# Optimization experiments

Measured on AMD Instinct MI355X. Metric: run time of the kernel, lower is better.

## Reference

```python
import jax, jax.numpy as jnp
import numpy as np

N_LAYERS, D_MODEL, H, D_K, D_V, D_FF, VOCAB = 6, 512, 8, 64, 64, 2048, 32000
B, S = 4, 512
NEG_INF = -jnp.inf


def positional_encoding(seq_len, d_model):
    # Faithful to the (buggy-vs-paper) source: angle = pos / 10000**(2*i/d_model),
    # sin for even i, cos for odd i (i is the raw channel index).
    pos = jnp.arange(seq_len, dtype=jnp.float32)[:, None]
    i = jnp.arange(d_model, dtype=jnp.float32)[None, :]
    angle = pos / jnp.power(10000.0, 2.0 * i / d_model)
    return jnp.where((jnp.arange(d_model) % 2 == 0)[None, :], jnp.sin(angle), jnp.cos(angle))


def layer_norm(x, g, b, eps=1e-5):
    mu = jnp.mean(x, -1, keepdims=True)
    var = jnp.mean((x - mu) ** 2, -1, keepdims=True)
    return (x - mu) * jax.lax.rsqrt(var + eps) * g + b


def mha(q_in, k_in, v_in, wq, wk, wv, wo, q_mask, k_mask, causal):
    # wq/wk: (H, D, D_K), wv: (H, D, D_V), wo: (H*D_V, D)
    q = jnp.einsum('bsd,hdk->bhsk', q_in, wq)
    k = jnp.einsum('btd,hdk->bhtk', k_in, wk)
    v = jnp.einsum('btd,hdk->bhtk', v_in, wv)
    scores = jnp.einsum('bhsk,bhtk->bhst', q, k) / jnp.sqrt(jnp.float32(D_K))
    allowed = q_mask[:, None, :, None] & k_mask[:, None, None, :]  # (B,1,S,T)
    if causal:
        sl, tl = q_in.shape[1], k_in.shape[1]
        allowed = allowed & (jnp.arange(tl)[None, :] <= jnp.arange(sl)[:, None])[None, None]
    scores = jnp.where(allowed, scores, NEG_INF)
    attn = jax.nn.softmax(scores, axis=-1)
    out = jnp.einsum('bhst,bhtk->bshk', attn, v)  # (B,S,H,D_V)
    out = out.reshape(out.shape[0], out.shape[1], H * D_V)
    return out @ wo


def ffn(x, w1, b1, w2, b2):
    return jax.nn.relu(x @ w1 + b1) @ w2 + b2


def setup_inputs() -> dict:
    key = jax.random.key(0)
    ks = iter(jax.random.split(key, 40))
    f = lambda shape, scale: (jax.random.normal(next(ks), shape, dtype=jnp.float32) * scale)
    inp = {
        'src_tokens': jax.random.randint(next(ks), (B, S), 0, VOCAB),
        'tgt_tokens': jax.random.randint(next(ks), (B, S), 0, VOCAB),
        'src_mask': jnp.ones((B, S), dtype=bool),
        'tgt_mask': jnp.ones((B, S), dtype=bool),
        'embed': f((VOCAB, D_MODEL), 0.02),
        'enc_wqkv': f((N_LAYERS, 3, H, D_MODEL, D_K), 0.04),
        'enc_wo': f((N_LAYERS, H * D_V, D_MODEL), 0.04),
        'enc_ff_w1': f((N_LAYERS, D_MODEL, D_FF), 0.02),
        'enc_ff_b1': jnp.zeros((N_LAYERS, D_FF), jnp.float32),
        'enc_ff_w2': f((N_LAYERS, D_FF, D_MODEL), 0.02),
        'enc_ff_b2': jnp.zeros((N_LAYERS, D_MODEL), jnp.float32),
        'enc_ln_g': jnp.ones((N_LAYERS, 2, D_MODEL), jnp.float32),
        'enc_ln_b': jnp.zeros((N_LAYERS, 2, D_MODEL), jnp.float32),
        'dec_wqkv1': f((N_LAYERS, 3, H, D_MODEL, D_K), 0.04),
        'dec_wo1': f((N_LAYERS, H * D_V, D_MODEL), 0.04),
        'dec_wqkv2': f((N_LAYERS, 3, H, D_MODEL, D_K), 0.04),
        'dec_wo2': f((N_LAYERS, H * D_V, D_MODEL), 0.04),
        'dec_ff_w1': f((N_LAYERS, D_MODEL, D_FF), 0.02),
        'dec_ff_b1': jnp.zeros((N_LAYERS, D_FF), jnp.float32),
        'dec_ff_w2': f((N_LAYERS, D_FF, D_MODEL), 0.02),
        'dec_ff_b2': jnp.zeros((N_LAYERS, D_MODEL), jnp.float32),
        'dec_ln_g': jnp.ones((N_LAYERS, 3, D_MODEL), jnp.float32),
        'dec_ln_b': jnp.zeros((N_LAYERS, 3, D_MODEL), jnp.float32),
        'out_w': f((D_MODEL, VOCAB), 0.02),
        'out_b': jnp.zeros((VOCAB,), jnp.float32),
    }
    return inp


def reference(src_tokens, tgt_tokens, src_mask, tgt_mask, embed,
              enc_wqkv, enc_wo, enc_ff_w1, enc_ff_b1, enc_ff_w2, enc_ff_b2, enc_ln_g, enc_ln_b,
              dec_wqkv1, dec_wo1, dec_wqkv2, dec_wo2, dec_ff_w1, dec_ff_b1, dec_ff_w2, dec_ff_b2,
              dec_ln_g, dec_ln_b, out_w, out_b):
    pe = positional_encoding(src_tokens.shape[1], D_MODEL)
    x = embed[src_tokens] + pe[None]
    for i in range(N_LAYERS):
        a = mha(x, x, x, enc_wqkv[i, 0], enc_wqkv[i, 1], enc_wqkv[i, 2], enc_wo[i], src_mask, src_mask, False)
        x = layer_norm(x + a, enc_ln_g[i, 0], enc_ln_b[i, 0])
        x = layer_norm(x + ffn(x, enc_ff_w1[i], enc_ff_b1[i], enc_ff_w2[i], enc_ff_b2[i]), enc_ln_g[i, 1], enc_ln_b[i, 1])
    pe_t = positional_encoding(tgt_tokens.shape[1], D_MODEL)
    y = embed[tgt_tokens] + pe_t[None]
    for i in range(N_LAYERS):
        a = mha(y, y, y, dec_wqkv1[i, 0], dec_wqkv1[i, 1], dec_wqkv1[i, 2], dec_wo1[i], tgt_mask, tgt_mask, True)
        y = layer_norm(y + a, dec_ln_g[i, 0], dec_ln_b[i, 0])
        a = mha(y, x, x, dec_wqkv2[i, 0], dec_wqkv2[i, 1], dec_wqkv2[i, 2], dec_wo2[i], tgt_mask, src_mask, False)
        y = layer_norm(y + a, dec_ln_g[i, 1], dec_ln_b[i, 1])
        y = layer_norm(y + ffn(y, dec_ff_w1[i], dec_ff_b1[i], dec_ff_w2[i], dec_ff_b2[i]), dec_ln_g[i, 2], dec_ln_b[i, 2])
    return y @ out_w + out_b
```

## Files before the change

### kernel.cpp

```cpp
#include <hip/hip_runtime.h>
#include <math.h>


typedef unsigned short u16;
typedef __attribute__((ext_vector_type(8))) short short8;
typedef __attribute__((ext_vector_type(4))) float f32x4;

__device__ __forceinline__ u16 f2bf(float f){
  unsigned u = __float_as_uint(f);
  return (u16)((u + 0x7fffu + ((u >> 16) & 1u)) >> 16);
}

#define GLDS16(gp, lp) __builtin_amdgcn_global_load_lds( \
    (const __attribute__((address_space(1))) unsigned int*)(const void*)(gp), \
    (__attribute__((address_space(3))) unsigned int*)(void*)(lp), 16, 0, 0)

__global__ __launch_bounds__(256) void embed_dual_kernel(
    const int* __restrict__ src, const int* __restrict__ tgt,
    const float* __restrict__ emb,
    float* __restrict__ xb, u16* __restrict__ xh,
    float* __restrict__ yb, u16* __restrict__ yh)
{
  int which = blockIdx.x >> 11;
  int row = blockIdx.x & 2047;
  int s = row & 511;
  int t = which ? tgt[row] : src[row];
  float* out = which ? yb : xb;
  u16*  outh = which ? yh : xh;
  #pragma unroll
  for (int j = 0; j < 2; j++){
    int d = threadIdx.x + 256*j;
    float ang = (float)s * powf(10000.0f, -2.0f*(float)d/512.0f);
    float pe = (d & 1) ? cosf(ang) : sinf(ang);
    float v = emb[(size_t)t*512 + d] + pe;
    out[(size_t)row*512 + d] = v;
    outh[(size_t)row*512 + d] = f2bf(v);
  }
}

struct WDesc { const float* W; unsigned long long gs, ds; u16* dst; int K; int nx; int end; };
struct WPack { WDesc d[6]; };

__device__ __forceinline__ void cast_body(const WPack& P, int nseg, int blk){
  __shared__ u16 T[64][65];
  int s = 0;
  while (s < nseg-1 && blk >= P.d[s].end) s++;
  WDesc D = P.d[s];
  int base = s ? P.d[s-1].end : 0;
  int lb = blk - base;
  int g = lb % D.nx, kt = lb / D.nx;
  int tid = threadIdx.x;
  const float* Wb = D.W + (size_t)g*D.gs + (size_t)kt*64*D.ds;
  #pragma unroll
  for (int i = 0; i < 16; i++){
    int li = tid + 256*i;
    int kk = li >> 6, c = li & 63;
    T[kk][c] = f2bf(Wb[(size_t)kk*D.ds + c]);
  }
  __syncthreads();
  #pragma unroll
  for (int i = 0; i < 16; i++){
    int lo = tid + 256*i;
    int c = lo >> 6, kk = lo & 63;
    D.dst[(size_t)(g*64 + c)*D.K + kt*64 + kk] = T[kk][c];
  }
}

__global__ __launch_bounds__(256) void wcast_multi(WPack P, int nseg){
  cast_body(P, nseg, blockIdx.x);
}

__device__ __forceinline__ void ln_body(
    float* __restrict__ x, const float* __restrict__ res,
    const float* __restrict__ g, const float* __restrict__ bt,
    u16* __restrict__ xh, int blk)
{
  int tid = threadIdx.x, lane = tid & 63, wv = tid >> 6;
  int row = blk*4 + wv;
  size_t base = (size_t)row*512;
  float v[8]; float sum = 0.f;
  #pragma unroll
  for (int j = 0; j < 8; j++){
    int d = lane + 64*j;
    v[j] = x[base + d] + res[base + d];
    sum += v[j];
  }
  #pragma unroll
  for (int o = 32; o; o >>= 1) sum += __shfl_xor(sum, o);
  float mu = sum * (1.0f/512.0f);
  float vs = 0.f;
  #pragma unroll
  for (int j = 0; j < 8; j++){ float dd = v[j] - mu; vs += dd*dd; }
  #pragma unroll
  for (int o = 32; o; o >>= 1) vs += __shfl_xor(vs, o);
  float rstd = rsqrtf(vs*(1.0f/512.0f) + 1e-5f);
  #pragma unroll
  for (int j = 0; j < 8; j++){
    int d = lane + 64*j;
    float ov = (v[j] - mu)*rstd*g[d] + bt[d];
    x[base + d] = ov;
    xh[base + d] = f2bf(ov);
  }
}

__global__ __launch_bounds__(256) void ln_cast_kernel(
    float* __restrict__ x, const float* __restrict__ res,
    const float* __restrict__ g, const float* __restrict__ bt,
    u16* __restrict__ xh, WPack P, int nseg)
{
  int bid = blockIdx.x;
  if (bid < 512){ ln_body(x, res, g, bt, xh, bid); return; }
  cast_body(P, nseg, bid - 512);
}

__global__ __launch_bounds__(256) void ln_kernel(
    float* __restrict__ x, const float* __restrict__ res,
    const float* __restrict__ g, const float* __restrict__ bt,
    u16* __restrict__ xh)
{
  ln_body(x, res, g, bt, xh, blockIdx.x);
}

__global__ __launch_bounds__(256) void flash_attn_kernel(
    const u16* __restrict__ qkv, const u16* __restrict__ vT,
    u16* __restrict__ ctx, int causal)
{
  __shared__ __align__(16) u16 lQ[64*64];
  __shared__ __align__(16) u16 lK[2][64*64];
  __shared__ __align__(16) u16 lV[2][64*64];
  __shared__ __align__(16) u16 lP[4][16*64];
  int tid = threadIdx.x, lane = tid & 63, w = tid >> 6;
  int r16 = lane & 15, l4 = lane >> 4;
  int bh = blockIdx.x >> 3, qb = blockIdx.x & 7;
  int b = bh >> 3, h = bh & 7;
  const u16* qbase = qkv + (size_t)b*512*1536 + h*64;

  #pragma unroll
  for (int i = 0; i < 2; i++){
    int idx = i*256 + tid;
    int r = idx >> 3, c = idx & 7;
    GLDS16(qbase + (size_t)(qb*64 + r)*1536 + ((c ^ (r & 7))*8),
           lQ + (i*256 + w*64)*8);
  }
  auto stageKV = [&](int buf, int tt){
    #pragma unroll
    for (int i = 0; i < 2; i++){
      int idx = i*256 + tid;
      int r = idx >> 3, c = idx & 7;
      GLDS16(qbase + 512 + (size_t)(tt*64 + r)*1536 + ((c ^ (r & 7))*8),
             lK[buf] + (i*256 + w*64)*8);
      GLDS16(vT + ((size_t)bh*64 + r)*512 + tt*64 + ((c ^ (r & 7))*8),
             lV[buf] + (i*256 + w*64)*8);
    }
  };
  stageKV(0, 0);
  __syncthreads();
  short8 qa[2];
  #pragma unroll
  for (int kt = 0; kt < 2; kt++){
    int q = w*16 + r16;
    qa[kt] = *(const short8*)&lQ[q*64 + (((kt*4 + l4) ^ (q & 7))*8)];
  }

  f32x4 o[4];
  float mrow[4], lrow[4];
  #pragma unroll
  for (int j = 0; j < 4; j++){ o[j] = (f32x4){0.f,0.f,0.f,0.f}; mrow[j] = -3e38f; lrow[j] = 0.f; }

  int ntl = causal ? (qb + 1) : 8;
  int buf = 0;
  for (int tt = 0; tt < ntl; tt++){
    if (tt + 1 < ntl) stageKV(buf ^ 1, tt + 1);
    f32x4 s[4];
    #pragma unroll
    for (int ct = 0; ct < 4; ct++) s[ct] = (f32x4){0.f,0.f,0.f,0.f};
    __builtin_amdgcn_s_setprio(1);
    #pragma unroll
    for (int kt = 0; kt < 2; kt++){
      #pragma unroll
      for (int ct = 0; ct < 4; ct++){
        int trow = ct*16 + r16;
        short8 kb = *(const short8*)&lK[buf][trow*64 + (((kt*4 + l4) ^ (trow & 7))*8)];
        s[ct] = __builtin_amdgcn_mfma_f32_16x16x32_bf16(qa[kt], kb, s[ct], 0, 0, 0);
      }
    }
    __builtin_amdgcn_s_setprio(0);
    float p[4][4];
    #pragma unroll
    for (int ct = 0; ct < 4; ct++)
      #pragma unroll
      for (int r = 0; r < 4; r++){
        float v = s[ct][r] * 0.125f;
        if (causal && tt == qb && (ct*16 + r16) > (w*16 + l4*4 + r)) v = -1e30f;
        p[ct][r] = v;
      }
    #pragma unroll
    for (int r = 0; r < 4; r++){
      float pm = fmaxf(fmaxf(p[0][r], p[1][r]), fmaxf(p[2][r], p[3][r]));
      #pragma unroll
      for (int off = 1; off < 16; off <<= 1) pm = fmaxf(pm, __shfl_xor(pm, off));
      float mn = fmaxf(mrow[r], pm);
      float scl = __expf(mrow[r] - mn);
      mrow[r] = mn;
      float rs = 0.f;
      #pragma unroll
      for (int ct = 0; ct < 4; ct++){ p[ct][r] = __expf(p[ct][r] - mn); rs += p[ct][r]; }
      #pragma unroll
      for (int off = 1; off < 16; off <<= 1) rs += __shfl_xor(rs, off);
      lrow[r] = lrow[r]*scl + rs;
      #pragma unroll
      for (int jf = 0; jf < 4; jf++) o[jf][r] *= scl;
    }
    u16* myP = &lP[w][0];
    #pragma unroll
    for (int ct = 0; ct < 4; ct++)
      #pragma unroll
      for (int r = 0; r < 4; r++){
        int q = l4*4 + r, t = ct*16 + r16;
        myP[q*64 + (((t >> 3) ^ (q & 7))*8) + (t & 7)] = f2bf(p[ct][r]);
      }
    __builtin_amdgcn_s_setprio(1);
    #pragma unroll
    for (int kt = 0; kt < 2; kt++){
      short8 pa = *(const short8*)&myP[r16*64 + (((kt*4 + l4) ^ (r16 & 7))*8)];
      #pragma unroll
      for (int jf = 0; jf < 4; jf++){
        int dr = jf*16 + r16;
        short8 vv = *(const short8*)&lV[buf][dr*64 + (((kt*4 + l4) ^ (dr & 7))*8)];
        o[jf] = __builtin_amdgcn_mfma_f32_16x16x32_bf16(pa, vv, o[jf], 0, 0, 0);
      }
    }
    __builtin_amdgcn_s_setprio(0);
    __syncthreads();
    buf ^= 1;
  }
  #pragma unroll
  for (int r = 0; r < 4; r++){
    float inv = 1.0f / lrow[r];
    int q = qb*64 + w*16 + l4*4 + r;
    u16* dst = ctx + (size_t)(b*512 + q)*512 + h*64;
    #pragma unroll
    for (int jf = 0; jf < 4; jf++)
      dst[jf*16 + r16] = f2bf(o[jf][r] * inv);
  }
}

template<int BM, int BN, int WM, int WN, int VOUT, int SWZ>
__global__ __launch_bounds__(WM*WN*64) void mfma_gemm(
    const u16* __restrict__ A, int lda,
    const u16* __restrict__ B, int ldb,
    void* __restrict__ C, int ldc, int cbf,
    const float* __restrict__ bias, int relu, int K, u16* __restrict__ vt)
{
  constexpr int NT  = WM*WN*64;
  constexpr int SM  = BM/WM, SN = BN/WN;
  constexpr int FM  = SM/16, FN = SN/16;
  constexpr int RPS = NT/8;
  constexpr int AG  = BM/RPS, BG = BN/RPS;
  __shared__ __align__(16) u16 lds[2][(BM+BN)*64];
  int bx, by;
  if constexpr (SWZ){
    int nwg = gridDim.x * gridDim.y;
    int lin = blockIdx.y * gridDim.x + blockIdx.x;
    int q = nwg >> 3, r = nwg & 7;
    int xcd = lin & 7, idx = lin >> 3;
    int wgid = (xcd < r ? xcd*(q+1) : r*(q+1) + (xcd-r)*q) + idx;
    bx = wgid / gridDim.y; by = wgid % gridDim.y;
  } else { bx = blockIdx.x; by = blockIdx.y; }
  int tid = threadIdx.x, lane = tid & 63, w = tid >> 6;
  int wm = w / WN, wn = w % WN;
  int r16 = lane & 15, l4 = lane >> 4;
  int sr = (w << 3) + (lane >> 3);
  int sc = lane & 7;
  int scs = sc ^ (sr & 7);
  const u16* Ab = A + (size_t)by*BM*lda + (size_t)sr*lda + scs*8;
  const u16* Bb = B + (size_t)bx*BN*ldb + (size_t)sr*ldb + scs*8;
  f32x4 acc[FM][FN];
  #pragma unroll
  for (int i = 0; i < FM; i++)
    #pragma unroll
    for (int j = 0; j < FN; j++)
      acc[i][j] = (f32x4){0.f, 0.f, 0.f, 0.f};

  auto stage = [&](int buf, int kt){
    #pragma unroll
    for (int s = 0; s < AG; s++)
      GLDS16(Ab + (size_t)(s*RPS)*lda + kt, &lds[buf][(s*RPS + (w << 3))*64]);
    #pragma unroll
    for (int s = 0; s < BG; s++)
      GLDS16(Bb + (size_t)(s*RPS)*ldb + kt, &lds[buf][(BM + s*RPS + (w << 3))*64]);
  };
  stage(0, 0);
  int nk = K >> 6, cur = 0;
  for (int kt = 0; kt < nk; kt++){
    __syncthreads();
    if (kt + 1 < nk) stage(cur ^ 1, (kt + 1) << 6);
    #pragma unroll
    for (int ks = 0; ks < 2; ks++){
      short8 av[FM], bv[FN];
      #pragma unroll
      for (int i = 0; i < FM; i++){
        int row = wm*SM + i*16 + r16;
        av[i] = *(const short8*)&lds[cur][row*64 + (((ks*4 + l4) ^ (row & 7))*8)];
      }
      #pragma unroll
      for (int j = 0; j < FN; j++){
        int row = wn*SN + j*16 + r16;
        bv[j] = *(const short8*)&lds[cur][(BM + row)*64 + (((ks*4 + l4) ^ (row & 7))*8)];
      }
      #pragma unroll
      for (int i = 0; i < FM; i++)
        #pragma unroll
        for (int j = 0; j < FN; j++)
          acc[i][j] = __builtin_amdgcn_mfma_f32_16x16x32_bf16(av[i], bv[j], acc[i][j], 0, 0, 0);
    }
    cur ^= 1;
  }

  if constexpr (VOUT){
    int nblk = bx * BN;
    if (nblk >= 1024){
      constexpr int TP = BM + 4;
      u16* T = &lds[0][0];
      __syncthreads();
      #pragma unroll
      for (int i = 0; i < FM; i++){
        int t0 = wm*SM + i*16 + l4*4;
        #pragma unroll
        for (int j = 0; j < FN; j++){
          int d = wn*SN + j*16 + r16;
          unsigned q01 = (unsigned)f2bf(acc[i][j][0]) | ((unsigned)f2bf(acc[i][j][1]) << 16);
          unsigned q23 = (unsigned)f2bf(acc[i][j][2]) | ((unsigned)f2bf(acc[i][j][3]) << 16);
          uint2 pk; pk.x = q01; pk.y = q23;
          *(uint2*)&T[d*TP + t0] = pk;
        }
      }
      __syncthreads();
      int h0 = (nblk - 1024) >> 6;
      int b = (by * BM) >> 9;
      int t0g = (by * BM) & 511;
      constexpr int U2PR = BM/4;
      constexpr int NIT = (BN*BM)/(NT*4);
      #pragma unroll
      for (int it = 0; it < NIT; it++){
        int idx = it*NT + tid;
        int d = idx / U2PR, tq = (idx % U2PR)*4;
        int hh = d >> 6, dd = d & 63;
        *(uint2*)&vt[((size_t)((b*8 + h0 + hh)*64 + dd))*512 + t0g + tq] =
            *(const uint2*)&T[d*TP + tq];
      }
      return;
    }
  }

  int m0 = by*BM + wm*SM, n0 = bx*BN + wn*SN;
  int r4 = l4*4;
  #pragma unroll
  for (int i = 0; i < FM; i++){
    #pragma unroll
    for (int j = 0; j < FN; j++){
      int col = n0 + j*16 + r16;
      float bi = bias ? bias[col] : 0.f;
      #pragma unroll
      for (int r = 0; r < 4; r++){
        int rowg = m0 + i*16 + r4 + r;
        float o = acc[i][j][r] + bi;
        if (relu) o = fmaxf(o, 0.f);
        if (cbf) ((u16*)C)[(size_t)rowg*ldc + col] = f2bf(o);
        else     ((float*)C)[(size_t)rowg*ldc + col] = o;
      }
    }
  }
}

__global__ __launch_bounds__(256) void xattn_qkv_gemm(
    const u16* __restrict__ Ay, const u16* __restrict__ Ax,
    const u16* __restrict__ Bt, u16* __restrict__ C, u16* __restrict__ vt)
{
  constexpr int BM=64, BN=64, WM=2, WN=2, NT=256;
  constexpr int SM=BM/WM, SN=BN/WN, FM=SM/16, FN=SN/16, RPS=NT/8;
  constexpr int AG=BM/RPS, BG=BN/RPS;
  __shared__ __align__(16) u16 lA[2][BM*64];
  __shared__ __align__(16) u16 lB[2][BN*64];
  int tid = threadIdx.x, lane = tid & 63, w = tid >> 6;
  int wm = w / WN, wn = w % WN;
  int r16 = lane & 15, l4 = lane >> 4;
  int sr = (w << 3) + (lane >> 3);
  int sc = lane & 7;
  int scs = sc ^ (sr & 7);
  int z = blockIdx.z;
  const u16* A = (z == 0) ? Ay : Ax;
  const u16* Ab = A + (size_t)blockIdx.y*BM*512 + (size_t)sr*512 + scs*8;
  const u16* Bb = Bt + (size_t)(z*512 + blockIdx.x*BN)*512 + (size_t)sr*512 + scs*8;
  f32x4 acc[FM][FN];
  #pragma unroll
  for (int i = 0; i < FM; i++)
    #pragma unroll
    for (int j = 0; j < FN; j++)
      acc[i][j] = (f32x4){0.f, 0.f, 0.f, 0.f};
  auto stage = [&](int buf, int kt){
    #pragma unroll
    for (int s = 0; s < AG; s++)
      GLDS16(Ab + (size_t)(s*RPS)*512 + kt, &lA[buf][(s*RPS + (w << 3))*64]);
    #pragma unroll
    for (int s = 0; s < BG; s++)
      GLDS16(Bb + (size_t)(s*RPS)*512 + kt, &lB[buf][(s*RPS + (w << 3))*64]);
  };
  stage(0, 0);
  int cur = 0;
  for (int kt = 0; kt < 8; kt++){
    __syncthreads();
    if (kt + 1 < 8) stage(cur ^ 1, (kt + 1) << 6);
    #pragma unroll
    for (int ks = 0; ks < 2; ks++){
      short8 av[FM], bv[FN];
      #pragma unroll
      for (int i = 0; i < FM; i++){
        int row = wm*SM + i*16 + r16;
        av[i] = *(const short8*)&lA[cur][row*64 + (((ks*4 + l4) ^ (row & 7))*8)];
      }
      #pragma unroll
      for (int j = 0; j < FN; j++){
        int row = wn*SN + j*16 + r16;
        bv[j] = *(const short8*)&lB[cur][row*64 + (((ks*4 + l4) ^ (row & 7))*8)];
      }
      #pragma unroll
      for (int i = 0; i < FM; i++)
        #pragma unroll
        for (int j = 0; j < FN; j++)
          acc[i][j] = __builtin_amdgcn_mfma_f32_16x16x32_bf16(av[i], bv[j], acc[i][j], 0, 0, 0);
    }
    cur ^= 1;
  }
  if (z == 2){
    constexpr int TP = BM + 4;
    u16* T = (u16*)&lA[0][0];
    __syncthreads();
    #pragma unroll
    for (int i = 0; i < FM; i++){
      int t0 = wm*SM + i*16 + l4*4;
      #pragma unroll
      for (int j = 0; j < FN; j++){
        int d = wn*SN + j*16 + r16;
        unsigned q01 = (unsigned)f2bf(acc[i][j][0]) | ((unsigned)f2bf(acc[i][j][1]) << 16);
        unsigned q23 = (unsigned)f2bf(acc[i][j][2]) | ((unsigned)f2bf(acc[i][j][3]) << 16);
        uint2 pk; pk.x = q01; pk.y = q23;
        *(uint2*)&T[d*TP + t0] = pk;
      }
    }
    __syncthreads();
    int h = blockIdx.x;
    int b = (blockIdx.y * BM) >> 9;
    int t0g = (blockIdx.y * BM) & 511;
    u16* dst = vt + (size_t)(b*8 + h)*64*512;
    #pragma unroll
    for (int it = 0; it < (BM*64)/(NT*4); it++){
      int idx = it*NT + tid;
      int d = idx >> 4, tq = (idx & 15)*4;
      *(uint2*)&dst[(size_t)d*512 + t0g + tq] = *(const uint2*)&T[d*TP + tq];
    }
    return;
  }
  int m0 = blockIdx.y*BM + wm*SM, n0 = z*512 + blockIdx.x*BN + wn*SN;
  int r4 = l4*4;
  #pragma unroll
  for (int i = 0; i < FM; i++)
    #pragma unroll
    for (int j = 0; j < FN; j++)
      #pragma unroll
      for (int r = 0; r < 4; r++){
        int rowg = m0 + i*16 + r4 + r;
        C[(size_t)rowg*1536 + n0 + j*16 + r16] = f2bf(acc[i][j][r]);
      }
}

extern "C" void kernel_launch(void* const* d_in, const int* in_sizes, int n_in,
                              void* d_out, int out_size, void* d_ws, size_t ws_size,
                              hipStream_t stream)
{
  (void)in_sizes; (void)n_in; (void)out_size; (void)ws_size;
  const int*   src_tok   = (const int*)  d_in[0];
  const int*   tgt_tok   = (const int*)  d_in[1];
  const float* emb       = (const float*)d_in[4];
  const float* enc_wqkv  = (const float*)d_in[5];
  const float* enc_wo    = (const float*)d_in[6];
  const float* enc_ff_w1 = (const float*)d_in[7];
  const float* enc_ff_b1 = (const float*)d_in[8];
  const float* enc_ff_w2 = (const float*)d_in[9];
  const float* enc_ff_b2 = (const float*)d_in[10];
  const float* enc_ln_g  = (const float*)d_in[11];
  const float* enc_ln_b  = (const float*)d_in[12];
  const float* dec_wqkv1 = (const float*)d_in[13];
  const float* dec_wo1   = (const float*)d_in[14];
  const float* dec_wqkv2 = (const float*)d_in[15];
  const float* dec_wo2   = (const float*)d_in[16];
  const float* dec_ff_w1 = (const float*)d_in[17];
  const float* dec_ff_b1 = (const float*)d_in[18];
  const float* dec_ff_w2 = (const float*)d_in[19];
  const float* dec_ff_b2 = (const float*)d_in[20];
  const float* dec_ln_g  = (const float*)d_in[21];
  const float* dec_ln_b  = (const float*)d_in[22];
  const float* out_w     = (const float*)d_in[23];
  const float* out_b     = (const float*)d_in[24];
  float* outp = (float*)d_out;

  const size_t MB = 1024*1024;
  char* wsb = (char*)d_ws;
  float* xb     = (float*)(wsb + 0*MB);
  u16*   sQKV2  = (u16*)  (wsb + 0*MB);
  u16*   sWO2   = (u16*)  (wsb + 1*MB + 512*1024);
  float* yb     = (float*)(wsb + 4*MB);
  u16*   xh     = (u16*)  (wsb + 8*MB);
  u16*   ctxb   = (u16*)  (wsb + 10*MB);
  u16*   yh     = (u16*)  (wsb + 12*MB);
  u16*   qkvb   = (u16*)  (wsb + 14*MB);
  u16*   vT     = (u16*)  (wsb + 20*MB);
  u16*   hid    = (u16*)  (wsb + 14*MB);
  u16*   sQKV   = (u16*)  (wsb + 22*MB);
  u16*   sWO    = (u16*)  (wsb + 23*MB + 512*1024);
  u16*   sFF1   = (u16*)  (wsb + 24*MB);
  u16*   sFF2   = (u16*)  (wsb + 26*MB);
  float* proj   = (float*)(wsb + 28*MB);
  u16*   wvbuf  = (u16*)  (wsb + 14*MB);

  auto g64 = [&](const u16* A,int lda,const u16* B,int ldb,void* C,int ldc,
                 int cbf,const float* bias,int relu,int M,int N,int K){
    mfma_gemm<64,64,2,2,0,0><<<dim3(N/64, M/64), 256, 0, stream>>>(
        A,lda,B,ldb,C,ldc,cbf,bias,relu,K,nullptr);
  };
  auto g128 = [&](const u16* A,int lda,const u16* B,int ldb,void* C,int ldc,
                  int cbf,const float* bias,int relu,int M,int N,int K){
    mfma_gemm<128,128,2,2,0,0><<<dim3(N/128, M/128), 256, 0, stream>>>(
        A,lda,B,ldb,C,ldc,cbf,bias,relu,K,nullptr);
  };
  auto gvocab = [&](const u16* A,const u16* B,void* C,int ldc,
                    const float* bias,int N){
    mfma_gemm<128,64,2,2,0,1><<<dim3(N/64, 16), 256, 0, stream>>>(
        A,512,B,512,C,ldc,0,bias,0,512,nullptr);
  };
  auto gqkv = [&](const u16* A,const u16* B,u16* C,u16* vt){
    mfma_gemm<128,128,2,2,1,0><<<dim3(12, 16), 256, 0, stream>>>(
        A,512,B,512,C,1536,1,nullptr,0,512,vt);
  };
  auto ln = [&](float* x, const float* g, const float* b, u16* oh){
    ln_kernel<<<512, 256, 0, stream>>>(x, proj, g, b, oh);
  };
  auto packof = [&](WDesc* segs, int n, int& tot){
    WPack P; tot = 0;
    for (int s = 0; s < n; s++){
      tot += segs[s].nx * (segs[s].K/64);
      segs[s].end = tot;
      P.d[s] = segs[s];
    }
    for (int s = n; s < 6; s++) P.d[s] = P.d[0];
    return P;
  };
  auto cast = [&](WDesc* segs, int n){
    int tot; WPack P = packof(segs, n, tot);
    wcast_multi<<<tot, 256, 0, stream>>>(P, n);
  };
  auto ln_cast = [&](float* x, const float* g, const float* b, u16* oh,
                     WDesc* segs, int n){
    int tot; WPack P = packof(segs, n, tot);
    ln_cast_kernel<<<512 + tot, 256, 0, stream>>>(x, proj, g, b, oh, P, n);
  };

  const size_t WQKV_L = (size_t)3*8*512*64;
  auto enc_segs = [&](int i, WDesc* s){
    s[0] = {enc_wqkv + i*WQKV_L,            32768, 64,   sQKV, 512,  24, 0};
    s[1] = {enc_wo   + (size_t)i*262144,    64,    512,  sWO,  512,  8,  0};
    s[2] = {enc_ff_w1+ (size_t)i*512*2048,  64,    2048, sFF1, 512,  32, 0};
    s[3] = {enc_ff_w2+ (size_t)i*2048*512,  64,    512,  sFF2, 2048, 8,  0};
  };
  auto dec_segs = [&](int i, WDesc* s){
    s[0] = {dec_wqkv1 + i*WQKV_L,           32768, 64,   sQKV,  512,  24, 0};
    s[1] = {dec_wo1   + (size_t)i*262144,   64,    512,  sWO,   512,  8,  0};
    s[2] = {dec_ff_w1 + (size_t)i*512*2048, 64,    2048, sFF1,  512,  32, 0};
    s[3] = {dec_ff_w2 + (size_t)i*2048*512, 64,    512,  sFF2,  2048, 8,  0};
    s[4] = {dec_wqkv2 + i*WQKV_L,           32768, 64,   sQKV2, 512,  24, 0};
    s[5] = {dec_wo2   + (size_t)i*262144,   64,    512,  sWO2,  512,  8,  0};
  };

  embed_dual_kernel<<<4096, 256, 0, stream>>>(src_tok, tgt_tok, emb, xb, xh, yb, yh);

  { WDesc s[4]; enc_segs(0, s); cast(s, 4); }
  for (int i = 0; i < 6; i++){
    gqkv(xh, sQKV, qkvb, vT);
    flash_attn_kernel<<<256, 256, 0, stream>>>(qkvb, vT, ctxb, 0);
    g64(ctxb, 512, sWO, 512, proj, 512, 0, nullptr, 0, 2048, 512, 512);
    ln(xb, enc_ln_g + i*1024, enc_ln_b + i*1024, xh);
    g128(xh, 512, sFF1, 512, hid, 2048, 1, enc_ff_b1 + i*2048, 1, 2048, 2048, 512);
    g64(hid, 2048, sFF2, 2048, proj, 512, 0, enc_ff_b2 + i*512, 0, 2048, 512, 2048);
    if (i < 5){
      WDesc s[4]; enc_segs(i+1, s);
      ln_cast(xb, enc_ln_g + i*1024 + 512, enc_ln_b + i*1024 + 512, xh, s, 4);
    } else {
      ln(xb, enc_ln_g + i*1024 + 512, enc_ln_b + i*1024 + 512, xh);
    }
  }

  { WDesc s[6]; dec_segs(0, s); cast(s, 6); }
  for (int i = 0; i < 6; i++){
    gqkv(yh, sQKV, qkvb, vT);
    flash_attn_kernel<<<256, 256, 0, stream>>>(qkvb, vT, ctxb, 1);
    g64(ctxb, 512, sWO, 512, proj, 512, 0, nullptr, 0, 2048, 512, 512);
    ln(yb, dec_ln_g + i*1536,        dec_ln_b + i*1536,        yh);
    xattn_qkv_gemm<<<dim3(8, 32, 3), 256, 0, stream>>>(yh, xh, sQKV2, qkvb, vT);
    flash_attn_kernel<<<256, 256, 0, stream>>>(qkvb, vT, ctxb, 0);
    g64(ctxb, 512, sWO2, 512, proj, 512, 0, nullptr, 0, 2048, 512, 512);
    ln(yb, dec_ln_g + i*1536 + 512,  dec_ln_b + i*1536 + 512,  yh);
    g128(yh, 512, sFF1, 512, hid, 2048, 1, dec_ff_b1 + i*2048, 1, 2048, 2048, 512);
    g64(hid, 2048, sFF2, 2048, proj, 512, 0, dec_ff_b2 + i*512, 0, 2048, 512, 2048);
    if (i < 5){
      WDesc s[6]; dec_segs(i+1, s);
      ln_cast(yb, dec_ln_g + i*1536 + 1024, dec_ln_b + i*1536 + 1024, yh, s, 6);
    } else {
      ln(yb, dec_ln_g + i*1536 + 1024, dec_ln_b + i*1536 + 1024, yh);
    }
  }

  for (int c = 0; c < 2; c++){
    int c0 = c*16000;
    WDesc seg[1] = {{out_w + c0, 64, 32000, wvbuf, 512, 250, 0}};
    cast(seg, 1);
    gvocab(yh, wvbuf, outp + c0, 32000, out_b + c0, 16000);
  }
}
```

Baseline: 1.403 ms.

## Split flash attention KV tiles across two wave groups with final softmax merge

The attention kernel now launches 512 threads per block, split into two groups of four waves. Each group processes alternating 64-key tiles for the same 64 queries, so the sequential KV loop per wave is roughly halved. The two partial softmax states (max, sum, output accumulators) are merged through LDS at the end. This doubles the KV staging buffers and adds a merge step and extra synchronisation, and with only 256 blocks it is meant to raise per-CU parallelism on the short attention loops.

```diff
diff --git a/kernel.cpp b/kernel.cpp
--- a/kernel.cpp
+++ b/kernel.cpp
@@ -121,44 +121,43 @@
   ln_body(x, res, g, bt, xh, blockIdx.x);
 }
 
-__global__ __launch_bounds__(256) void flash_attn_kernel(
+__global__ __launch_bounds__(512) void flash_attn_kernel(
     const u16* __restrict__ qkv, const u16* __restrict__ vT,
     u16* __restrict__ ctx, int causal)
 {
   __shared__ __align__(16) u16 lQ[64*64];
-  __shared__ __align__(16) u16 lK[2][64*64];
-  __shared__ __align__(16) u16 lV[2][64*64];
-  __shared__ __align__(16) u16 lP[4][16*64];
+  __shared__ __align__(16) u16 lK[4][64*64];
+  __shared__ __align__(16) u16 lV[4][64*64];
+  __shared__ __align__(16) u16 lP[8][16*64];
   int tid = threadIdx.x, lane = tid & 63, w = tid >> 6;
+  int g = w >> 2, wl = w & 3;
   int r16 = lane & 15, l4 = lane >> 4;
   int bh = blockIdx.x >> 3, qb = blockIdx.x & 7;
   int b = bh >> 3, h = bh & 7;
   const u16* qbase = qkv + (size_t)b*512*1536 + h*64;
-
-  #pragma unroll
-  for (int i = 0; i < 2; i++){
-    int idx = i*256 + tid;
-    int r = idx >> 3, c = idx & 7;
-    GLDS16(qbase + (size_t)(qb*64 + r)*1536 + ((c ^ (r & 7))*8),
-           lQ + (i*256 + w*64)*8);
-  }
-  auto stageKV = [&](int buf, int tt){
-    #pragma unroll
-    for (int i = 0; i < 2; i++){
-      int idx = i*256 + tid;
-      int r = idx >> 3, c = idx & 7;
-      GLDS16(qbase + 512 + (size_t)(tt*64 + r)*1536 + ((c ^ (r & 7))*8),
-             lK[buf] + (i*256 + w*64)*8);
-      GLDS16(vT + ((size_t)bh*64 + r)*512 + tt*64 + ((c ^ (r & 7))*8),
-             lV[buf] + (i*256 + w*64)*8);
-    }
-  };
-  stageKV(0, 0);
+  int sr = tid >> 3, sc = tid & 7;
+
+  GLDS16(qbase + (size_t)(qb*64 + sr)*1536 + ((sc ^ (sr & 7))*8),
+         lQ + (w << 6)*8);
+  auto stageK = [&](int buf, int tt){
+    GLDS16(qbase + 512 + (size_t)(tt*64 + sr)*1536 + ((sc ^ (sr & 7))*8),
+           lK[buf] + (w << 6)*8);
+  };
+  auto stageV = [&](int buf, int tt){
+    GLDS16(vT + ((size_t)bh*64 + sr)*512 + tt*64 + ((sc ^ (sr & 7))*8),
+           lV[buf] + (w << 6)*8);
+  };
+
+  int ntl = causal ? (qb + 1) : 8;
+  int nrounds = (ntl + 1) >> 1;
+  stageK(0, 0); stageV(0, 0);
+  if (ntl > 1){ stageK(1, 1); stageV(1, 1); }
   __syncthreads();
+
   short8 qa[2];
   #pragma unroll
   for (int kt = 0; kt < 2; kt++){
-    int q = w*16 + r16;
+    int q = wl*16 + r16;
     qa[kt] = *(const short8*)&lQ[q*64 + (((kt*4 + l4) ^ (q & 7))*8)];
   }
 
@@ -167,81 +166,107 @@
   #pragma unroll
   for (int j = 0; j < 4; j++){ o[j] = (f32x4){0.f,0.f,0.f,0.f}; mrow[j] = -3e38f; lrow[j] = 0.f; }
 
-  int ntl = causal ? (qb + 1) : 8;
-  int buf = 0;
-  for (int tt = 0; tt < ntl; tt++){
-    if (tt + 1 < ntl) stageKV(buf ^ 1, tt + 1);
-    f32x4 s[4];
-    #pragma unroll
-    for (int ct = 0; ct < 4; ct++) s[ct] = (f32x4){0.f,0.f,0.f,0.f};
-    __builtin_amdgcn_s_setprio(1);
-    #pragma unroll
-    for (int kt = 0; kt < 2; kt++){
-      #pragma unroll
-      for (int ct = 0; ct < 4; ct++){
-        int trow = ct*16 + r16;
-        short8 kb = *(const short8*)&lK[buf][trow*64 + (((kt*4 + l4) ^ (trow & 7))*8)];
-        s[ct] = __builtin_amdgcn_mfma_f32_16x16x32_bf16(qa[kt], kb, s[ct], 0, 0, 0);
-      }
-    }
-    __builtin_amdgcn_s_setprio(0);
-    float p[4][4];
-    #pragma unroll
-    for (int ct = 0; ct < 4; ct++)
+  for (int rd = 0; rd < nrounds; rd++){
+    if (rd > 0) __syncthreads();
+    if (rd + 1 < nrounds){
+      int base = ((rd + 1) & 1)*2;
+      int t0 = 2*(rd + 1);
+      stageK(base, t0); stageV(base, t0);
+      if (t0 + 1 < ntl){ stageK(base + 1, t0 + 1); stageV(base + 1, t0 + 1); }
+    }
+    int tr = 2*rd + g;
+    if (tr < ntl){
+      int buf = (rd & 1)*2 + g;
+      f32x4 s[4];
+      #pragma unroll
+      for (int ct = 0; ct < 4; ct++) s[ct] = (f32x4){0.f,0.f,0.f,0.f};
+      __builtin_amdgcn_s_setprio(1);
+      #pragma unroll
+      for (int kt = 0; kt < 2; kt++){
+        #pragma unroll
+        for (int ct = 0; ct < 4; ct++){
+          int trow = ct*16 + r16;
+          short8 kb = *(const short8*)&lK[buf][trow*64 + (((kt*4 + l4) ^ (trow & 7))*8)];
+          s[ct] = __builtin_amdgcn_mfma_f32_16x16x32_bf16(qa[kt], kb, s[ct], 0, 0, 0);
+        }
+      }
+      __builtin_amdgcn_s_setprio(0);
+      float p[4][4];
+      #pragma unroll
+      for (int ct = 0; ct < 4; ct++)
+        #pragma unroll
+        for (int r = 0; r < 4; r++){
+          float v = s[ct][r] * 0.125f;
+          if (causal && tr == qb && (ct*16 + r16) > (wl*16 + l4*4 + r)) v = -1e30f;
+          p[ct][r] = v;
+        }
       #pragma unroll
       for (int r = 0; r < 4; r++){
-        float v = s[ct][r] * 0.125f;
-        if (causal && tt == qb && (ct*16 + r16) > (w*16 + l4*4 + r)) v = -1e30f;
-        p[ct][r] = v;
-      }
+        float pm = fmaxf(fmaxf(p[0][r], p[1][r]), fmaxf(p[2][r], p[3][r]));
+        #pragma unroll
+        for (int off = 1; off < 16; off <<= 1) pm = fmaxf(pm, __shfl_xor(pm, off));
+        float mn = fmaxf(mrow[r], pm);
+        float scl = __expf(mrow[r] - mn);
+        mrow[r] = mn;
+        float rs = 0.f;
+        #pragma unroll
+        for (int ct = 0; ct < 4; ct++){ p[ct][r] = __expf(p[ct][r] - mn); rs += p[ct][r]; }
+        #pragma unroll
+        for (int off = 1; off < 16; off <<= 1) rs += __shfl_xor(rs, off);
+        lrow[r] = lrow[r]*scl + rs;
+        #pragma unroll
+        for (int jf = 0; jf < 4; jf++) o[jf][r] *= scl;
+      }
+      u16* myP = &lP[w][0];
+      #pragma unroll
+      for (int ct = 0; ct < 4; ct++)
+        #pragma unroll
+        for (int r = 0; r < 4; r++){
+          int q = l4*4 + r, t = ct*16 + r16;
+          myP[q*64 + (((t >> 3) ^ (q & 7))*8) + (t & 7)] = f2bf(p[ct][r]);
+        }
+      __builtin_amdgcn_s_setprio(1);
+      #pragma unroll
+      for (int kt = 0; kt < 2; kt++){
+        short8 pa = *(const short8*)&myP[r16*64 + (((kt*4 + l4) ^ (r16 & 7))*8)];
+        #pragma unroll
+        for (int jf = 0; jf < 4; jf++){
+          int dr = jf*16 + r16;
+          short8 vv = *(const short8*)&lV[buf][dr*64 + (((kt*4 + l4) ^ (dr & 7))*8)];
+          o[jf] = __builtin_amdgcn_mfma_f32_16x16x32_bf16(pa, vv, o[jf], 0, 0, 0);
+        }
+      }
+      __builtin_amdgcn_s_setprio(0);
+    }
+  }
+
+  __syncthreads();
+  float* mrg = (float*)&lK[0][0];
+  if (w >= 4){
+    float* p = mrg + ((size_t)(wl*64 + lane))*25;
+    #pragma unroll
+    for (int r = 0; r < 4; r++){ p[r] = mrow[r]; p[4 + r] = lrow[r]; }
+    #pragma unroll
+    for (int jf = 0; jf < 4; jf++)
+      #pragma unroll
+      for (int r = 0; r < 4; r++) p[8 + jf*4 + r] = o[jf][r];
+  }
+  __syncthreads();
+  if (w < 4){
+    float* p = mrg + ((size_t)(w*64 + lane))*25;
     #pragma unroll
     for (int r = 0; r < 4; r++){
-      float pm = fmaxf(fmaxf(p[0][r], p[1][r]), fmaxf(p[2][r], p[3][r]));
-      #pragma unroll
-      for (int off = 1; off < 16; off <<= 1) pm = fmaxf(pm, __shfl_xor(pm, off));
-      float mn = fmaxf(mrow[r], pm);
-      float scl = __expf(mrow[r] - mn);
-      mrow[r] = mn;
-      float rs = 0.f;
-      #pragma unroll
-      for (int ct = 0; ct < 4; ct++){ p[ct][r] = __expf(p[ct][r] - mn); rs += p[ct][r]; }
-      #pragma unroll
-      for (int off = 1; off < 16; off <<= 1) rs += __shfl_xor(rs, off);
-      lrow[r] = lrow[r]*scl + rs;
-      #pragma unroll
-      for (int jf = 0; jf < 4; jf++) o[jf][r] *= scl;
-    }
-    u16* myP = &lP[w][0];
-    #pragma unroll
-    for (int ct = 0; ct < 4; ct++)
-      #pragma unroll
-      for (int r = 0; r < 4; r++){
-        int q = l4*4 + r, t = ct*16 + r16;
-        myP[q*64 + (((t >> 3) ^ (q & 7))*8) + (t & 7)] = f2bf(p[ct][r]);
-      }
-    __builtin_amdgcn_s_setprio(1);
-    #pragma unroll
-    for (int kt = 0; kt < 2; kt++){
-      short8 pa = *(const short8*)&myP[r16*64 + (((kt*4 + l4) ^ (r16 & 7))*8)];
-      #pragma unroll
-      for (int jf = 0; jf < 4; jf++){
-        int dr = jf*16 + r16;
-        short8 vv = *(const short8*)&lV[buf][dr*64 + (((kt*4 + l4) ^ (dr & 7))*8)];
-        o[jf] = __builtin_amdgcn_mfma_f32_16x16x32_bf16(pa, vv, o[jf], 0, 0, 0);
-      }
-    }
-    __builtin_amdgcn_s_setprio(0);
-    __syncthreads();
-    buf ^= 1;
-  }
-  #pragma unroll
-  for (int r = 0; r < 4; r++){
-    float inv = 1.0f / lrow[r];
-    int q = qb*64 + w*16 + l4*4 + r;
-    u16* dst = ctx + (size_t)(b*512 + q)*512 + h*64;
-    #pragma unroll
-    for (int jf = 0; jf < 4; jf++)
-      dst[jf*16 + r16] = f2bf(o[jf][r] * inv);
+      float m1 = p[r], l1 = p[4 + r];
+      float M  = fmaxf(mrow[r], m1);
+      float s0 = __expf(mrow[r] - M), s1 = __expf(m1 - M);
+      float L  = lrow[r]*s0 + l1*s1;
+      float inv = 1.0f / L;
+      int q = qb*64 + w*16 + l4*4 + r;
+      u16* dst = ctx + (size_t)(b*512 + q)*512 + h*64;
+      #pragma unroll
+      for (int jf = 0; jf < 4; jf++)
+        dst[jf*16 + r16] = f2bf((o[jf][r]*s0 + p[8 + jf*4 + r]*s1) * inv);
+    }
   }
 }
 
@@ -586,7 +611,7 @@
   { WDesc s[4]; enc_segs(0, s); cast(s, 4); }
   for (int i = 0; i < 6; i++){
     gqkv(xh, sQKV, qkvb, vT);
-    flash_attn_kernel<<<256, 256, 0, stream>>>(qkvb, vT, ctxb, 0);
+    flash_attn_kernel<<<256, 512, 0, stream>>>(qkvb, vT, ctxb, 0);
     g64(ctxb, 512, sWO, 512, proj, 512, 0, nullptr, 0, 2048, 512, 512);
     ln(xb, enc_ln_g + i*1024, enc_ln_b + i*1024, xh);
     g128(xh, 512, sFF1, 512, hid, 2048, 1, enc_ff_b1 + i*2048, 1, 2048, 2048, 512);
@@ -602,11 +627,11 @@
   { WDesc s[6]; dec_segs(0, s); cast(s, 6); }
   for (int i = 0; i < 6; i++){
     gqkv(yh, sQKV, qkvb, vT);
-    flash_attn_kernel<<<256, 256, 0, stream>>>(qkvb, vT, ctxb, 1);
+    flash_attn_kernel<<<256, 512, 0, stream>>>(qkvb, vT, ctxb, 1);
     g64(ctxb, 512, sWO, 512, proj, 512, 0, nullptr, 0, 2048, 512, 512);
     ln(yb, dec_ln_g + i*1536,        dec_ln_b + i*1536,        yh);
     xattn_qkv_gemm<<<dim3(8, 32, 3), 256, 0, stream>>>(yh, xh, sQKV2, qkvb, vT);
-    flash_attn_kernel<<<256, 256, 0, stream>>>(qkvb, vT, ctxb, 0);
+    flash_attn_kernel<<<256, 512, 0, stream>>>(qkvb, vT, ctxb, 0);
     g64(ctxb, 512, sWO2, 512, proj, 512, 0, nullptr, 0, 2048, 512, 512);
     ln(yb, dec_ln_g + i*1536 + 512,  dec_ln_b + i*1536 + 512,  yh);
     g128(yh, 512, sFF1, 512, hid, 2048, 1, dec_ff_b1 + i*2048, 1, 2048, 2048, 512);
```

Result: faster. 1.343 ms (-4.3%).
